# Kernel optimization log

Hardware: AMD Instinct MI355X
Metric: run time of the kernel (lower is better)

Reference implementation:

```python
import jax, jax.numpy as jnp
import numpy as np

B, H, W, C = 8, 64, 64, 768
NH, HD = 12, 64          # num_heads, head_dim
WS = 16                  # window size
SCALE = HD ** -0.5


def setup_inputs() -> dict:
    key = jax.random.key(0)
    ks = jax.random.split(key, 6)
    x = jax.random.normal(ks[0], (B, H * W, C), dtype=jnp.float32)
    w_qkv = jax.random.normal(ks[1], (3 * C, C), dtype=jnp.float32) * 0.02
    w_out = jax.random.normal(ks[2], (C, C), dtype=jnp.float32) * 0.02
    b_out = jnp.zeros((C,), dtype=jnp.float32)
    rel_pos_h = jax.random.normal(ks[3], (2 * WS - 1, HD), dtype=jnp.float32) * 0.02
    rel_pos_w = jax.random.normal(ks[4], (2 * WS - 1, HD), dtype=jnp.float32) * 0.02
    return {"x": x, "w_qkv": w_qkv, "w_out": w_out, "b_out": b_out,
            "rel_pos_h": rel_pos_h, "rel_pos_w": rel_pos_w}


def reference(x, w_qkv, w_out, b_out, rel_pos_h, rel_pos_w):
    nh_w, nw_w = H // WS, W // WS
    xw = x.reshape(B, nh_w, WS, nw_w, WS, C).transpose(0, 1, 3, 2, 4, 5)
    Bw = B * nh_w * nw_w
    t = WS * WS
    xw = xw.reshape(Bw, t, C)

    # ---- qkv projection (no bias) and rearrange 'b t (qkv l d) -> qkv b l t d'
    qkv = (xw @ w_qkv.T).reshape(Bw, t, 3, NH, HD).transpose(2, 0, 3, 1, 4)
    q, k, v = qkv[0], qkv[1], qkv[2]        # each (Bw, NH, t, HD)

    # ---- scaled attention scores
    att = jnp.einsum('bhxd,bhyd->bhxy', q, k) * SCALE   # (Bw, NH, t, t)

    # ---- decomposed relative position bias (SAM/MViT style, q_size == k_size == WS)
    idx = jnp.arange(WS)[:, None] - jnp.arange(WS)[None, :] + (WS - 1)  # (WS, WS)
    Rh = rel_pos_h[idx]                      # (WS, WS, HD)
    Rw = rel_pos_w[idx]                      # (WS, WS, HD)
    rq = q.reshape(Bw * NH, WS, WS, HD)
    rel_h = jnp.einsum('bhwc,hkc->bhwk', rq, Rh)   # (Bw*NH, WS, WS, WS)
    rel_w = jnp.einsum('bhwc,wkc->bhwk', rq, Rw)
    att = (att.reshape(Bw * NH, WS, WS, WS, WS)
           + rel_h[:, :, :, :, None]
           + rel_w[:, :, :, None, :]).reshape(Bw, NH, t, t)

    # ---- softmax + AV
    att = jax.nn.softmax(att, axis=-1)
    o = jnp.einsum('bhxy,bhyd->bhxd', att, v)          # (Bw, NH, t, HD)
    o = o.transpose(0, 2, 1, 3).reshape(Bw, t, C)      # 'b h l d -> b l (h d)'

    # ---- output projection
    o = o @ w_out.T + b_out

    # ---- window unpartition back to (B, H*W, C)
    o = o.reshape(B, nh_w, nw_w, WS, WS, C).transpose(0, 1, 3, 2, 4, 5)
    return o.reshape(B, H * W, C)
```

## Files before the change

### kernel.cpp

```cpp
#include <hip/hip_runtime.h>

typedef __attribute__((ext_vector_type(8))) short bf16x8;
typedef __attribute__((ext_vector_type(4))) float f32x4;
typedef unsigned short u16;

__device__ __forceinline__ u16 f2bf(float f) {
  union { float f; unsigned u; } v; v.f = f;
  unsigned r = v.u + 0x7fffu + ((v.u >> 16) & 1u);
  return (u16)(r >> 16);
}
__device__ __forceinline__ float bf2f(u16 u) {
  union { unsigned u; float f; } v; v.u = ((unsigned)u) << 16;
  return v.f;
}
__device__ __forceinline__ void gload16(const void* g, void* l) {
  __builtin_amdgcn_global_load_lds((const __attribute__((address_space(1))) void*)g,
                                   (__attribute__((address_space(3))) void*)l, 16, 0, 0);
}

__global__ void sab_cvt_kernel(const float* __restrict__ src, u16* __restrict__ dst, int n4) {
  int i = blockIdx.x * blockDim.x + threadIdx.x;
  if (i >= n4) return;
  float4 f = reinterpret_cast<const float4*>(src)[i];
  ushort4 o; o.x = f2bf(f.x); o.y = f2bf(f.y); o.z = f2bf(f.z); o.w = f2bf(f.w);
  reinterpret_cast<ushort4*>(dst)[i] = o;
}

__global__ void sab_xw_kernel(const float* __restrict__ x, u16* __restrict__ xw) {
  const int r = blockIdx.x;
  const int w = r >> 8, tt = r & 255;
  const int b = w >> 4, h1 = (w >> 2) & 3, w1 = w & 3;
  const int i = tt >> 4, j = tt & 15;
  const long xrow = (long)b * 4096 + (h1 * 16 + i) * 64 + w1 * 16 + j;
  const float4* src = reinterpret_cast<const float4*>(x + xrow * 768);
  ushort4* dst = reinterpret_cast<ushort4*>(xw + (long)r * 768);
  const int c = threadIdx.x;
  float4 f = src[c];
  ushort4 o; o.x = f2bf(f.x); o.y = f2bf(f.y); o.z = f2bf(f.z); o.w = f2bf(f.w);
  dst[c] = o;
}

template<int EPI>
__global__ __launch_bounds__(256, 4)
void sab_gemm_kernel(const u16* __restrict__ A, const u16* __restrict__ Bt,
                     u16* __restrict__ outB, u16* __restrict__ vTp,
                     float* __restrict__ outF, const float* __restrict__ bias,
                     const int K, const int N)
{
  __shared__ __align__(16) u16 Ash[128 * 64];
  __shared__ __align__(16) u16 Bsh[128 * 64];
  const int tid = threadIdx.x;
  const int lane = tid & 63, wid = tid >> 6;
  const int wr = wid >> 1, wc = wid & 1;
  const int lr = lane & 15, lg = lane >> 4;
  const long m0 = (long)blockIdx.x * 128;
  const long n0 = (long)blockIdx.y * 128;

  const int srow = tid >> 3;
  const int scol = (tid & 7) * 8;
  const u16* Ag = A + (m0 + srow) * K + scol;
  const u16* Bg = Bt + (n0 + srow) * K + scol;
  u16* Al = Ash + wid * 512;
  u16* Bl = Bsh + wid * 512;

  f32x4 acc[4][4];
#pragma unroll
  for (int a = 0; a < 4; ++a)
#pragma unroll
    for (int b = 0; b < 4; ++b) acc[a][b] = (f32x4){0.f, 0.f, 0.f, 0.f};

  for (int kt = 0; kt < K; kt += 64) {
#pragma unroll
    for (int i = 0; i < 4; ++i) {
      gload16(Ag + (long)i * 32 * K + kt, Al + i * 2048);
      gload16(Bg + (long)i * 32 * K + kt, Bl + i * 2048);
    }
    __syncthreads();
    bf16x8 af[4][2], bfr[4][2];
#pragma unroll
    for (int mt = 0; mt < 4; ++mt)
#pragma unroll
      for (int kc = 0; kc < 2; ++kc)
        af[mt][kc] = *reinterpret_cast<const bf16x8*>(&Ash[(wr * 64 + mt * 16 + lr) * 64 + kc * 32 + lg * 8]);
#pragma unroll
    for (int nt = 0; nt < 4; ++nt)
#pragma unroll
      for (int kc = 0; kc < 2; ++kc)
        bfr[nt][kc] = *reinterpret_cast<const bf16x8*>(&Bsh[(wc * 64 + nt * 16 + lr) * 64 + kc * 32 + lg * 8]);
#pragma unroll
    for (int kc = 0; kc < 2; ++kc)
#pragma unroll
      for (int mt = 0; mt < 4; ++mt)
#pragma unroll
        for (int nt = 0; nt < 4; ++nt)
          acc[mt][nt] = __builtin_amdgcn_mfma_f32_16x16x32_bf16(af[mt][kc], bfr[nt][kc], acc[mt][nt], 0, 0, 0);
    __syncthreads();
  }

#pragma unroll
  for (int mt = 0; mt < 4; ++mt)
#pragma unroll
    for (int nt = 0; nt < 4; ++nt) {
      const long col = n0 + wc * 64 + nt * 16 + lr;
      if (EPI == 0) {
        const long row0 = m0 + wr * 64 + mt * 16 + lg * 4;
        if (n0 < 1536) {
#pragma unroll
          for (int r = 0; r < 4; ++r)
            outB[(row0 + r) * 1536 + col] = f2bf(acc[mt][nt][r]);
        } else {
          ushort4 o;
          o.x = f2bf(acc[mt][nt][0]); o.y = f2bf(acc[mt][nt][1]);
          o.z = f2bf(acc[mt][nt][2]); o.w = f2bf(acc[mt][nt][3]);
          *reinterpret_cast<ushort4*>(&vTp[(col - 1536) * 32768L + row0]) = o;
        }
      } else {
        const float bv = bias[col];
#pragma unroll
        for (int r = 0; r < 4; ++r) {
          const int rr = (int)(m0 + wr * 64 + mt * 16 + lg * 4 + r);
          const int w = rr >> 8, tt = rr & 255;
          const long xrow = (long)(w >> 4) * 4096 + (((w >> 2) & 3) * 16 + (tt >> 4)) * 64 + (w & 3) * 16 + (tt & 15);
          outF[xrow * 768 + col] = acc[mt][nt][r] + bv;
        }
      }
    }
}

__global__ __launch_bounds__(256, 2)
void sab_attn_kernel(const u16* __restrict__ qk, const u16* __restrict__ vT,
                     const float* __restrict__ rph, const float* __restrict__ rpw,
                     u16* __restrict__ oatt)
{
  __shared__ __align__(16) u16 relh_s[256 * 16];
  __shared__ __align__(16) u16 relw_s[256 * 16];
  __shared__ __align__(16) u16 Sbuf[4][64 * 72];

  const int blk0 = blockIdx.x;
  const int blk = (blk0 & 7) * 192 + (blk0 >> 3);
  const int w = blk / 12, h = blk % 12;
  const long qbase = (long)w * 256;
  const int tid = threadIdx.x, lane = tid & 63, wid = tid >> 6;
  const int lr = lane & 15, lg = lane >> 4;

  const u16* Qp = qk + (long)h * 64;
  const u16* Kp = qk + 768 + (long)h * 64;
  const u16* Vt = vT + (long)h * 64 * 32768 + w * 256;

#pragma unroll
  for (int ii = 0; ii < 4; ++ii) {
    const int i = wid * 4 + ii;
    f32x4 acc = (f32x4){0.f, 0.f, 0.f, 0.f};
#pragma unroll
    for (int kc = 0; kc < 2; ++kc) {
      bf16x8 a = *reinterpret_cast<const bf16x8*>(&Qp[(qbase + i * 16 + lr) * 1536 + kc * 32 + lg * 8]);
      const float* bp = rph + (i - lr + 15) * 64 + kc * 32 + lg * 8;
      bf16x8 b;
#pragma unroll
      for (int e = 0; e < 8; ++e) b[e] = (short)f2bf(bp[e]);
      acc = __builtin_amdgcn_mfma_f32_16x16x32_bf16(a, b, acc, 0, 0, 0);
    }
#pragma unroll
    for (int r = 0; r < 4; ++r)
      relh_s[(i * 16 + lg * 4 + r) * 16 + lr] = f2bf(acc[r]);
  }
#pragma unroll
  for (int jj = 0; jj < 4; ++jj) {
    const int j = wid * 4 + jj;
    f32x4 acc = (f32x4){0.f, 0.f, 0.f, 0.f};
#pragma unroll
    for (int kc = 0; kc < 2; ++kc) {
      bf16x8 a = *reinterpret_cast<const bf16x8*>(&Qp[(qbase + lr * 16 + j) * 1536 + kc * 32 + lg * 8]);
      const float* bp = rpw + (j - lr + 15) * 64 + kc * 32 + lg * 8;
      bf16x8 b;
#pragma unroll
      for (int e = 0; e < 8; ++e) b[e] = (short)f2bf(bp[e]);
      acc = __builtin_amdgcn_mfma_f32_16x16x32_bf16(a, b, acc, 0, 0, 0);
    }
#pragma unroll
    for (int r = 0; r < 4; ++r)
      relw_s[((lg * 4 + r) * 16 + j) * 16 + lr] = f2bf(acc[r]);
  }
  __syncthreads();

  bf16x8 qa[4][2];
#pragma unroll
  for (int mt = 0; mt < 4; ++mt)
#pragma unroll
    for (int kc = 0; kc < 2; ++kc)
      qa[mt][kc] = *reinterpret_cast<const bf16x8*>(&Qp[(qbase + wid * 64 + mt * 16 + lr) * 1536 + kc * 32 + lg * 8]);

  float rw[4][4];
#pragma unroll
  for (int mt = 0; mt < 4; ++mt)
#pragma unroll
    for (int r = 0; r < 4; ++r)
      rw[mt][r] = bf2f(relw_s[(wid * 64 + mt * 16 + lg * 4 + r) * 16 + lr]);

  float mrun[4][4], lrun[4][4];
  f32x4 oacc[4][4];
#pragma unroll
  for (int mt = 0; mt < 4; ++mt)
#pragma unroll
    for (int r = 0; r < 4; ++r) { mrun[mt][r] = -1e30f; lrun[mt][r] = 0.f; }
#pragma unroll
  for (int mt = 0; mt < 4; ++mt)
#pragma unroll
    for (int nt = 0; nt < 4; ++nt) oacc[mt][nt] = (f32x4){0.f, 0.f, 0.f, 0.f};

  u16* sb = &Sbuf[wid][0];

  for (int kb = 0; kb < 4; ++kb) {
    bf16x8 kf[4][2], vf[4][2];
#pragma unroll
    for (int nt = 0; nt < 4; ++nt)
#pragma unroll
      for (int kc = 0; kc < 2; ++kc) {
        kf[nt][kc] = *reinterpret_cast<const bf16x8*>(&Kp[(qbase + kb * 64 + nt * 16 + lr) * 1536 + kc * 32 + lg * 8]);
        vf[nt][kc] = *reinterpret_cast<const bf16x8*>(&Vt[(nt * 16 + lr) * 32768L + kb * 64 + kc * 32 + lg * 8]);
      }

#pragma unroll
    for (int mt = 0; mt < 4; ++mt) {
      f32x4 sn[4];
#pragma unroll
      for (int nt = 0; nt < 4; ++nt) {
        f32x4 t = (f32x4){0.f, 0.f, 0.f, 0.f};
#pragma unroll
        for (int kc = 0; kc < 2; ++kc)
          t = __builtin_amdgcn_mfma_f32_16x16x32_bf16(qa[mt][kc], kf[nt][kc], t, 0, 0, 0);
        sn[nt] = t;
      }
#pragma unroll
      for (int r = 0; r < 4; ++r) {
        const int x = wid * 64 + mt * 16 + lg * 4 + r;
        float sv[4];
#pragma unroll
        for (int nt = 0; nt < 4; ++nt)
          sv[nt] = sn[nt][r] * 0.125f + bf2f(relh_s[x * 16 + kb * 4 + nt]) + rw[mt][r];
        float rmax = fmaxf(fmaxf(sv[0], sv[1]), fmaxf(sv[2], sv[3]));
        rmax = fmaxf(rmax, __shfl_xor(rmax, 1));
        rmax = fmaxf(rmax, __shfl_xor(rmax, 2));
        rmax = fmaxf(rmax, __shfl_xor(rmax, 4));
        rmax = fmaxf(rmax, __shfl_xor(rmax, 8));
        const float mnew = fmaxf(mrun[mt][r], rmax);
        const float sf = __expf(mrun[mt][r] - mnew);
        mrun[mt][r] = mnew;
        float rsum = 0.f;
#pragma unroll
        for (int nt = 0; nt < 4; ++nt) { const float p = __expf(sv[nt] - mnew); sv[nt] = p; rsum += p; }
        rsum += __shfl_xor(rsum, 1);
        rsum += __shfl_xor(rsum, 2);
        rsum += __shfl_xor(rsum, 4);
        rsum += __shfl_xor(rsum, 8);
        lrun[mt][r] = lrun[mt][r] * sf + rsum;
#pragma unroll
        for (int nt = 0; nt < 4; ++nt) oacc[mt][nt][r] *= sf;
        const int rowl = mt * 16 + lg * 4 + r;
#pragma unroll
        for (int nt = 0; nt < 4; ++nt) sb[rowl * 72 + nt * 16 + lr] = f2bf(sv[nt]);
      }
    }

#pragma unroll
    for (int kc = 0; kc < 2; ++kc)
#pragma unroll
      for (int mt = 0; mt < 4; ++mt) {
        bf16x8 pa = *reinterpret_cast<const bf16x8*>(&sb[(mt * 16 + lr) * 72 + kc * 32 + lg * 8]);
#pragma unroll
        for (int nt = 0; nt < 4; ++nt)
          oacc[mt][nt] = __builtin_amdgcn_mfma_f32_16x16x32_bf16(pa, vf[nt][kc], oacc[mt][nt], 0, 0, 0);
      }
  }

#pragma unroll
  for (int mt = 0; mt < 4; ++mt)
#pragma unroll
    for (int r = 0; r < 4; ++r) {
      const float inv = 1.f / lrun[mt][r];
      const long row = qbase + wid * 64 + mt * 16 + lg * 4 + r;
#pragma unroll
      for (int nt = 0; nt < 4; ++nt)
        oatt[row * 768 + h * 64 + nt * 16 + lr] = f2bf(oacc[mt][nt][r] * inv);
    }
}

extern "C" void kernel_launch(void* const* d_in, const int* in_sizes, int n_in,
                              void* d_out, int out_size, void* d_ws, size_t ws_size,
                              hipStream_t stream) {
  (void)in_sizes; (void)n_in; (void)out_size; (void)ws_size;
  const float* x     = (const float*)d_in[0];
  const float* w_qkv = (const float*)d_in[1];
  const float* w_out = (const float*)d_in[2];
  const float* b_out = (const float*)d_in[3];
  const float* rph   = (const float*)d_in[4];
  const float* rpw   = (const float*)d_in[5];
  float* out = (float*)d_out;

  char* ws = (char*)d_ws;
  u16* qk    = (u16*)ws;
  u16* vT    = (u16*)(ws + 100663296L);
  u16* xw    = (u16*)(ws + 150994944L);
  u16* wqkvb = (u16*)(ws + 201326592L);
  u16* woutb = (u16*)(ws + 204865536L);
  u16* oatt  = xw;

  sab_cvt_kernel<<<dim3(1728), dim3(256), 0, stream>>>(w_qkv, wqkvb, 442368);
  sab_cvt_kernel<<<dim3(576), dim3(256), 0, stream>>>(w_out, woutb, 147456);
  sab_xw_kernel<<<dim3(32768), dim3(192), 0, stream>>>(x, xw);
  sab_gemm_kernel<0><<<dim3(256, 18), dim3(256), 0, stream>>>(xw, wqkvb, qk, vT, nullptr, nullptr, 768, 2304);
  sab_attn_kernel<<<dim3(1536), dim3(256), 0, stream>>>(qk, vT, rph, rpw, oatt);
  sab_gemm_kernel<1><<<dim3(256, 6), dim3(256), 0, stream>>>(oatt, woutb, nullptr, nullptr, out, b_out, 768, 768);
}
```

Baseline: 366.4 us.

## Rewrite GEMMs as 256x256-tile 8-wave double-buffered pipelined kernel with swizzled LDS

```diff
diff --git a/kernel.cpp b/kernel.cpp
--- a/kernel.cpp
+++ b/kernel.cpp
@@ -17,6 +17,10 @@
   __builtin_amdgcn_global_load_lds((const __attribute__((address_space(1))) void*)g,
                                    (__attribute__((address_space(3))) void*)l, 16, 0, 0);
 }
+
+#define PH_BAR __builtin_amdgcn_s_barrier()
+#define LGKM0  asm volatile("s_waitcnt lgkmcnt(0)" ::: "memory")
+#define VM6    asm volatile("s_waitcnt vmcnt(6)" ::: "memory")
 
 __global__ void sab_cvt_kernel(const float* __restrict__ src, u16* __restrict__ dst, int n4) {
   int i = blockIdx.x * blockDim.x + threadIdx.x;
@@ -41,69 +45,109 @@
 }
 
 template<int EPI>
-__global__ __launch_bounds__(256, 4)
-void sab_gemm_kernel(const u16* __restrict__ A, const u16* __restrict__ Bt,
-                     u16* __restrict__ outB, u16* __restrict__ vTp,
-                     float* __restrict__ outF, const float* __restrict__ bias,
-                     const int K, const int N)
+__global__ __launch_bounds__(512, 2)
+void sab_gemm8_kernel(const u16* __restrict__ A, const u16* __restrict__ Bt,
+                      u16* __restrict__ outB, u16* __restrict__ vTp,
+                      float* __restrict__ outF, const float* __restrict__ bias,
+                      const int K)
 {
-  __shared__ __align__(16) u16 Ash[128 * 64];
-  __shared__ __align__(16) u16 Bsh[128 * 64];
+  __shared__ __align__(16) u16 lds[2][2][2][8192];
   const int tid = threadIdx.x;
   const int lane = tid & 63, wid = tid >> 6;
-  const int wr = wid >> 1, wc = wid & 1;
+  const int wr = wid >> 2, wc = wid & 3;
   const int lr = lane & 15, lg = lane >> 4;
-  const long m0 = (long)blockIdx.x * 128;
-  const long n0 = (long)blockIdx.y * 128;
-
-  const int srow = tid >> 3;
-  const int scol = (tid & 7) * 8;
-  const u16* Ag = A + (m0 + srow) * K + scol;
-  const u16* Bg = Bt + (n0 + srow) * K + scol;
-  u16* Al = Ash + wid * 512;
-  u16* Bl = Bsh + wid * 512;
-
-  f32x4 acc[4][4];
-#pragma unroll
-  for (int a = 0; a < 4; ++a)
+
+  const int nwg = gridDim.x * gridDim.y;
+  const int bid0 = blockIdx.y * gridDim.x + blockIdx.x;
+  const int bid = (bid0 & 7) * (nwg >> 3) + (bid0 >> 3);
+  const long m0 = (long)(bid % gridDim.x) * 256;
+  const long n0 = (long)(bid / gridDim.x) * 256;
+
+  const int swz = ((lane & 7) ^ (lane >> 3)) << 3;
+  const u16* Agl = A  + (m0 + wid * 8 + (lane >> 3)) * (long)K + swz;
+  const u16* Bgl = Bt + (n0 + wid * 8 + (lane >> 3)) * (long)K + swz;
+
+  f32x4 acc[8][4];
+#pragma unroll
+  for (int a = 0; a < 8; ++a)
 #pragma unroll
     for (int b = 0; b < 4; ++b) acc[a][b] = (f32x4){0.f, 0.f, 0.f, 0.f};
 
-  for (int kt = 0; kt < K; kt += 64) {
-#pragma unroll
-    for (int i = 0; i < 4; ++i) {
-      gload16(Ag + (long)i * 32 * K + kt, Al + i * 2048);
-      gload16(Bg + (long)i * 32 * K + kt, Bl + i * 2048);
-    }
-    __syncthreads();
-    bf16x8 af[4][2], bfr[4][2];
-#pragma unroll
-    for (int mt = 0; mt < 4; ++mt)
+  auto stage = [&](int buf, int mat, int half, int rb, int kt) {
+    const u16* g = (mat ? Bgl : Agl) + (half * 128 + rb) * (long)K + kt;
+    gload16(g, &lds[buf][mat][half][(rb + wid * 8) * 64]);
+  };
+  auto rdA4 = [&](int buf, int q, bf16x8 (&out)[4][2]) {
+#pragma unroll
+    for (int m2 = 0; m2 < 4; ++m2)
 #pragma unroll
       for (int kc = 0; kc < 2; ++kc)
-        af[mt][kc] = *reinterpret_cast<const bf16x8*>(&Ash[(wr * 64 + mt * 16 + lr) * 64 + kc * 32 + lg * 8]);
-#pragma unroll
-    for (int nt = 0; nt < 4; ++nt)
+        out[m2][kc] = *reinterpret_cast<const bf16x8*>(
+          &lds[buf][0][wr][(q * 64 + m2 * 16 + lr) * 64 + ((kc * 32 + lg * 8) ^ ((lr & 7) << 3))]);
+  };
+  auto rdB2 = [&](int buf, int q, bf16x8 (&out)[2][2]) {
+#pragma unroll
+    for (int n2 = 0; n2 < 2; ++n2)
 #pragma unroll
       for (int kc = 0; kc < 2; ++kc)
-        bfr[nt][kc] = *reinterpret_cast<const bf16x8*>(&Bsh[(wc * 64 + nt * 16 + lr) * 64 + kc * 32 + lg * 8]);
+        out[n2][kc] = *reinterpret_cast<const bf16x8*>(
+          &lds[buf][1][wc >> 1][((wc & 1) * 64 + q * 32 + n2 * 16 + lr) * 64 + ((kc * 32 + lg * 8) ^ ((lr & 7) << 3))]);
+  };
+  auto mma16 = [&](bf16x8 (&a)[4][2], bf16x8 (&b)[2][2], int mq, int nq) {
+    __builtin_amdgcn_s_setprio(1);
 #pragma unroll
     for (int kc = 0; kc < 2; ++kc)
 #pragma unroll
-      for (int mt = 0; mt < 4; ++mt)
-#pragma unroll
-        for (int nt = 0; nt < 4; ++nt)
-          acc[mt][nt] = __builtin_amdgcn_mfma_f32_16x16x32_bf16(af[mt][kc], bfr[nt][kc], acc[mt][nt], 0, 0, 0);
-    __syncthreads();
+      for (int m2 = 0; m2 < 4; ++m2)
+#pragma unroll
+        for (int n2 = 0; n2 < 2; ++n2)
+          acc[mq * 4 + m2][nq * 2 + n2] = __builtin_amdgcn_mfma_f32_16x16x32_bf16(
+              a[m2][kc], b[n2][kc], acc[mq * 4 + m2][nq * 2 + n2], 0, 0, 0);
+    __builtin_amdgcn_s_setprio(0);
+  };
+
+  stage(0,0,0,0,0);  stage(0,0,1,0,0);  stage(0,1,0,0,0);  stage(0,1,1,0,0);
+  stage(0,1,0,64,0); stage(0,1,1,64,0); stage(0,0,0,64,0); stage(0,0,1,64,0);
+  stage(1,0,0,0,64); stage(1,0,1,0,64); stage(1,1,0,0,64); stage(1,1,1,0,64);
+  stage(1,1,0,64,64); stage(1,1,1,64,64);
+  VM6; PH_BAR;
+
+  bf16x8 af[4][2], b0[2][2], b1[2][2];
+
+  for (int kt = 0; kt < K; kt += 128) {
+    const int k2 = kt + 128, k3 = kt + 192;
+    const bool s2 = k2 < K, s3 = k3 < K;
+    rdA4(0, 0, af); rdB2(0, 0, b0);
+    stage(1,0,0,64, kt + 64); stage(1,0,1,64, kt + 64);
+    PH_BAR; LGKM0; mma16(af, b0, 0, 0); PH_BAR;
+    rdB2(0, 1, b1);
+    if (s2) { stage(0,0,0,0, k2); stage(0,0,1,0, k2); }
+    PH_BAR; LGKM0; mma16(af, b1, 0, 1); PH_BAR;
+    rdA4(0, 1, af);
+    if (s2) { stage(0,1,0,0, k2); stage(0,1,1,0, k2); }
+    PH_BAR; LGKM0; mma16(af, b0, 1, 0); PH_BAR;
+    if (s2) { stage(0,1,0,64, k2); stage(0,1,1,64, k2); }
+    PH_BAR; mma16(af, b1, 1, 1); VM6; PH_BAR;
+    rdA4(1, 0, af); rdB2(1, 0, b0);
+    if (s2) { stage(0,0,0,64, k2); stage(0,0,1,64, k2); }
+    PH_BAR; LGKM0; mma16(af, b0, 0, 0); PH_BAR;
+    rdB2(1, 1, b1);
+    if (s3) { stage(1,0,0,0, k3); stage(1,0,1,0, k3); }
+    PH_BAR; LGKM0; mma16(af, b1, 0, 1); PH_BAR;
+    rdA4(1, 1, af);
+    if (s3) { stage(1,1,0,0, k3); stage(1,1,1,0, k3); }
+    PH_BAR; LGKM0; mma16(af, b0, 1, 0); PH_BAR;
+    if (s3) { stage(1,1,0,64, k3); stage(1,1,1,64, k3); }
+    PH_BAR; mma16(af, b1, 1, 1); VM6; PH_BAR;
   }
 
 #pragma unroll
-  for (int mt = 0; mt < 4; ++mt)
+  for (int mt = 0; mt < 8; ++mt)
 #pragma unroll
     for (int nt = 0; nt < 4; ++nt) {
       const long col = n0 + wc * 64 + nt * 16 + lr;
+      const long row0 = m0 + wr * 128 + mt * 16 + lg * 4;
       if (EPI == 0) {
-        const long row0 = m0 + wr * 64 + mt * 16 + lg * 4;
         if (n0 < 1536) {
 #pragma unroll
           for (int r = 0; r < 4; ++r)
@@ -118,7 +162,7 @@
         const float bv = bias[col];
 #pragma unroll
         for (int r = 0; r < 4; ++r) {
-          const int rr = (int)(m0 + wr * 64 + mt * 16 + lg * 4 + r);
+          const int rr = (int)(row0 + r);
           const int w = rr >> 8, tt = rr & 255;
           const long xrow = (long)(w >> 4) * 4096 + (((w >> 2) & 3) * 16 + (tt >> 4)) * 64 + (w & 3) * 16 + (tt & 15);
           outF[xrow * 768 + col] = acc[mt][nt][r] + bv;
@@ -308,7 +352,7 @@
   sab_cvt_kernel<<<dim3(1728), dim3(256), 0, stream>>>(w_qkv, wqkvb, 442368);
   sab_cvt_kernel<<<dim3(576), dim3(256), 0, stream>>>(w_out, woutb, 147456);
   sab_xw_kernel<<<dim3(32768), dim3(192), 0, stream>>>(x, xw);
-  sab_gemm_kernel<0><<<dim3(256, 18), dim3(256), 0, stream>>>(xw, wqkvb, qk, vT, nullptr, nullptr, 768, 2304);
+  sab_gemm8_kernel<0><<<dim3(128, 9), dim3(512), 0, stream>>>(xw, wqkvb, qk, vT, nullptr, nullptr, 768);
   sab_attn_kernel<<<dim3(1536), dim3(256), 0, stream>>>(qk, vT, rph, rpw, oatt);
-  sab_gemm_kernel<1><<<dim3(256, 6), dim3(256), 0, stream>>>(oatt, woutb, nullptr, nullptr, out, b_out, 768, 768);
-}
+  sab_gemm8_kernel<1><<<dim3(128, 3), dim3(512), 0, stream>>>(oatt, woutb, nullptr, nullptr, out, b_out, 768);
+}
```

New measurement: 371.7 us. Within noise of the previous version (+1.4%).
